# Kernel optimization log

Hardware: AMD Instinct MI355X
Metric: run time of the kernel (lower is better)

## Reference

```python
import jax, jax.numpy as jnp
import numpy as np

B, E, H, LEVELS, MAXN = 16, 256, 256, 12, 2
N = 2 ** LEVELS - 1  # 4095 nodes, level-order perfect binary tree
NODE_VOCAB, EDGE_VOCAB = 64, 128

PARAM_SHAPES = {
    'node_emb': (NODE_VOCAB, E), 'edge_emb': (EDGE_VOCAB, E),
    'bu_Wioux': (E, 3 * H), 'bu_bioux': (3 * H,), 'bu_Wfx': (E, H), 'bu_bfx': (H,),
    'bu_Wiouh': (MAXN * H, 3 * H), 'bu_Wfh': (MAXN, MAXN * H, H),
    'bu_eWih': (E, 4 * H), 'bu_eWhh': (H, 4 * H), 'bu_ebih': (4 * H,), 'bu_ebhh': (4 * H,),
    'td_Wioux': (E, 3 * H), 'td_bioux': (3 * H,), 'td_Wfx': (E, H), 'td_bfx': (H,),
    'td_Wiouhc': (MAXN * H, 3 * H), 'td_Wiouhp': (H, 3 * H),
    'td_Wfchild': (MAXN, (MAXN + 1) * H, H), 'td_Wfparent': ((MAXN + 1) * H, H),
    'td_eWih': (E, 4 * H), 'td_eWhh': (H, 4 * H), 'td_ebih': (4 * H,), 'td_ebhh': (4 * H,),
}
FLOAT_NAMES = list(PARAM_SHAPES)

_sig = jax.nn.sigmoid

def _lstm(x, h, c, Wih, Whh, bih, bhh):
    # torch nn.LSTMCell gate order: i, f, g, o
    g = x @ Wih + h @ Whh + bih + bhh
    i, f, gg, o = jnp.split(g, 4, axis=-1)
    c2 = _sig(f) * c + _sig(i) * jnp.tanh(gg)
    return _sig(o) * jnp.tanh(c2), c2

def _forward(p, node_ids, edge_ids):
    x_all = p['node_emb'][node_ids]  # [B,N,E]
    e_all = p['edge_emb'][edge_ids]  # [B,N,E] edge to parent
    bu_h = [None] * LEVELS
    bu_he = [None] * LEVELS
    bu_ce = [None] * LEVELS
    # ---- bottom-up n-ary TreeLSTM, level by level (deepest first) ----
    for l in range(LEVELS - 1, -1, -1):
        M = 2 ** l
        s = M - 1
        x = x_all[:, s:s + M]
        if l == LEVELS - 1:  # leaves: zero-padded children (no fc terms)
            ch_h = jnp.zeros((B, M, MAXN, H), x.dtype)
            ch_c = ch_h
        else:
            ch_h = bu_he[l + 1].reshape(B, M, MAXN, H)
            ch_c = bu_ce[l + 1].reshape(B, M, MAXN, H)
        cat = ch_h.reshape(B, M, MAXN * H)  # child_cat_h
        iou = x @ p['bu_Wioux'] + p['bu_bioux'] + cat @ p['bu_Wiouh']
        i, o, u = jnp.split(iou, 3, axis=-1)
        i, o, u = _sig(i), _sig(o), jnp.tanh(u)
        fx = x @ p['bu_Wfx'] + p['bu_bfx']
        f = _sig(fx[:, :, None, :] + jnp.einsum('bmc,kch->bmkh', cat, p['bu_Wfh']))
        c = i * u + (f * ch_c).sum(axis=2)
        h = o * jnp.tanh(c)
        bu_h[l] = h
        # edge-transition LSTMCell before passing state to parent
        he, ce = _lstm(e_all[:, s:s + M], h, c, p['bu_eWih'], p['bu_eWhh'], p['bu_ebih'], p['bu_ebhh'])
        bu_he[l] = he
        bu_ce[l] = ce
    # ---- top-down n-ary TreeLSTM (root first) ----
    td_h = [None] * LEVELS
    ph = jnp.zeros((B, 1, H), x_all.dtype)
    pc = ph
    for l in range(LEVELS):
        M = 2 ** l
        s = M - 1
        x = x_all[:, s:s + M]
        if l == LEVELS - 1:
            ch_h = jnp.zeros((B, M, MAXN, H), x.dtype)
            ch_c = ch_h
        else:
            ch_h = bu_he[l + 1].reshape(B, M, MAXN, H)
            ch_c = bu_ce[l + 1].reshape(B, M, MAXN, H)
        cat = ch_h.reshape(B, M, MAXN * H)
        iou = x @ p['td_Wioux'] + p['td_bioux'] + cat @ p['td_Wiouhc'] + ph @ p['td_Wiouhp']
        i, o, u = jnp.split(iou, 3, axis=-1)
        i, o, u = _sig(i), _sig(o), jnp.tanh(u)
        fx = x @ p['td_Wfx'] + p['td_bfx']
        pcat = jnp.concatenate([ph, cat], axis=-1)  # [B,M,(MAXN+1)H]
        f_ch = _sig(fx[:, :, None, :] + jnp.einsum('bmc,kch->bmkh', pcat, p['td_Wfchild']))
        f_par = _sig(fx + pcat @ p['td_Wfparent'])
        c = i * u + (f_ch * ch_c).sum(axis=2) + f_par * pc
        h = o * jnp.tanh(c)
        td_h[l] = h
        if l < LEVELS - 1:
            M2 = 2 * M
            s2 = 2 * M - 1
            ph_r = jnp.repeat(h, 2, axis=1)
            pc_r = jnp.repeat(c, 2, axis=1)
            ph, pc = _lstm(e_all[:, s2:s2 + M2], ph_r, pc_r, p['td_eWih'], p['td_eWhh'], p['td_ebih'], p['td_ebhh'])
    return jnp.concatenate([jnp.concatenate(bu_h, 1), jnp.concatenate(td_h, 1)], axis=-1)  # [B,N,2H]


def setup_inputs() -> dict:
    key = jax.random.key(0)
    ks = jax.random.split(key, len(PARAM_SHAPES) + 2)
    inp = {}
    for k, (name, shp) in zip(ks, PARAM_SHAPES.items()):
        inp[name] = jax.random.normal(k, shp, dtype=jnp.float32) * 0.05
    inp['node_ids'] = jax.random.randint(ks[-2], (B, N), 0, NODE_VOCAB)
    inp['edge_ids'] = jax.random.randint(ks[-1], (B, N), 0, EDGE_VOCAB)
    return inp


def reference(node_emb, edge_emb, bu_Wioux, bu_bioux, bu_Wfx, bu_bfx, bu_Wiouh, bu_Wfh,
              bu_eWih, bu_eWhh, bu_ebih, bu_ebhh, td_Wioux, td_bioux, td_Wfx, td_bfx,
              td_Wiouhc, td_Wiouhp, td_Wfchild, td_Wfparent, td_eWih, td_eWhh, td_ebih, td_ebhh,
              node_ids, edge_ids):
    floats = (node_emb, edge_emb, bu_Wioux, bu_bioux, bu_Wfx, bu_bfx, bu_Wiouh, bu_Wfh,
              bu_eWih, bu_eWhh, bu_ebih, bu_ebhh, td_Wioux, td_bioux, td_Wfx, td_bfx,
              td_Wiouhc, td_Wiouhp, td_Wfchild, td_Wfparent, td_eWih, td_eWhh, td_ebih, td_ebhh)
    return _forward(dict(zip(FLOAT_NAMES, floats)), node_ids, edge_ids)
```

## Files before the change

kernel.cpp:

```cpp
#include <hip/hip_runtime.h>
#include <math.h>

#define NB 16
#define NH 256
#define NLV 12
#define NN 4095
#define OUTW 512

typedef unsigned short u16;
typedef __attribute__((ext_vector_type(4))) float f32x4;
typedef __attribute__((ext_vector_type(8))) short bf16x8;

__device__ __forceinline__ float sigf(float x){ return 1.0f/(1.0f + expf(-x)); }

__device__ __forceinline__ u16 f2bf(float x){
  unsigned int u = __float_as_uint(x);
  return (u16)((u + 0x7fffu + ((u >> 16) & 1u)) >> 16);
}
__device__ __forceinline__ float bf2f(u16 h){
  return __uint_as_float(((unsigned int)h) << 16);
}

__device__ __forceinline__ void gload16(const void* g, void* l){
  __builtin_amdgcn_global_load_lds(
      (const __attribute__((address_space(1))) unsigned int*)g,
      (__attribute__((address_space(3))) unsigned int*)l, 16, 0, 0);
}

template<int VAR, int NG>
__global__ __launch_bounds__(256, (NG >= 5 ? 2 : 3)) void fused_gemm(
    int R, int logM, int s,
    const int* __restrict__ ids,
    const u16* __restrict__ emb,
    const u16* __restrict__ hsrc,
    const u16* __restrict__ hsrc2,
    const u16* __restrict__ Wth, int wstride,
    const float* __restrict__ bias,
    const float* __restrict__ cce,
    const float* __restrict__ cprev,
    float* __restrict__ c_out,
    u16* __restrict__ h_out,
    float* __restrict__ out)
{
  constexpr int K0 = 256;
  constexpr int K1 = (VAR == 0) ? (NG == 5 ? 512 : 0) : 256;
  constexpr int K2 = (VAR == 2 && NG == 6) ? 512 : 0;
  constexpr int KTOT = K0 + K1 + K2;

  __shared__ u16 As[128][64];
  __shared__ u16 Bs[NG * 32][64];

  int tid = threadIdx.x, lane = tid & 63, w = tid >> 6;
  int wrow = w >> 1, whh = w & 1;
  int hh0 = blockIdx.y * 32;
  int M = 1 << logM;

  int lrow8 = lane >> 3;
  int gran  = lane & 7;
  int swz = (gran ^ lrow8) * 8;

  const u16* pa0[4]; const u16* pa1[4]; const u16* pa2[4];
  #pragma unroll
  for (int c = 0; c < 4; ++c){
    int gr = blockIdx.x * 128 + c * 32 + w * 8 + lrow8;
    if (gr > R - 1) gr = R - 1;
    int b = gr >> logM, m = gr & (M - 1);
    int j = s + m;
    pa0[c] = emb + (size_t)ids[b * NN + j] * 256 + swz;
    if constexpr (K1 > 0){
      if constexpr (VAR == 0)
        pa1[c] = hsrc + ((size_t)(b * NN + 2 * j + 1)) * NH + swz;
      else if constexpr (VAR == 3)
        pa1[c] = hsrc + ((size_t)(b * (M >> 1) + (m >> 1))) * NH + swz;
      else
        pa1[c] = hsrc + (size_t)gr * NH + swz;
    }
    if constexpr (K2 > 0)
      pa2[c] = hsrc2 + ((size_t)(b * NN + 2 * j + 1)) * NH + swz;
  }
  const u16* pb = Wth + (size_t)(hh0 + w * 8 + lrow8) * wstride + swz;

  f32x4 acc[NG][4];
  #pragma unroll
  for (int g = 0; g < NG; ++g)
    #pragma unroll
    for (int i = 0; i < 4; ++i) acc[g][i] = (f32x4)0.0f;

  for (int kt = 0; kt < KTOT; kt += 64){
    __syncthreads();
    #pragma unroll
    for (int c = 0; c < 4; ++c){
      const u16* ga;
      if (kt < K0) ga = pa0[c] + kt;
      else if (K1 > 0 && kt < K0 + K1) ga = pa1[c] + (kt - K0);
      else ga = pa2[c] + (kt - K0 - K1);
      gload16(ga, &As[c * 32 + w * 8][0]);
    }
    #pragma unroll
    for (int g = 0; g < NG; ++g)
      gload16(pb + (size_t)g * 256 * wstride + kt, &Bs[g * 32 + w * 8][0]);
    __syncthreads();

    #pragma unroll
    for (int kc = 0; kc < 2; ++kc){
      int g2 = ((kc * 4 + (lane >> 4)) ^ (lane & 7)) * 8;
      bf16x8 a[4];
      #pragma unroll
      for (int i = 0; i < 4; ++i)
        a[i] = *(const bf16x8*)&As[wrow * 64 + i * 16 + (lane & 15)][g2];
      bf16x8 bf[NG];
      #pragma unroll
      for (int g = 0; g < NG; ++g)
        bf[g] = *(const bf16x8*)&Bs[g * 32 + whh * 16 + (lane & 15)][g2];
      #pragma unroll
      for (int g = 0; g < NG; ++g)
        #pragma unroll
        for (int i = 0; i < 4; ++i)
          acc[g][i] = __builtin_amdgcn_mfma_f32_16x16x32_bf16(a[i], bf[g], acc[g][i], 0, 0, 0);
    }
  }

  int hhL = hh0 + whh * 16 + (lane & 15);
  float bb[NG];
  #pragma unroll
  for (int g = 0; g < NG; ++g) bb[g] = bias[g * 256 + hhL];

  #pragma unroll
  for (int i = 0; i < 4; ++i){
    #pragma unroll
    for (int r = 0; r < 4; ++r){
      int row = blockIdx.x * 128 + wrow * 64 + i * 16 + ((lane >> 4) << 2) + r;
      if (row >= R) continue;
      int b = row >> logM, m = row & (M - 1);
      int j = s + m;
      if constexpr (VAR == 0){
        float iv = sigf(acc[0][i][r] + bb[0]);
        float ov = sigf(acc[1][i][r] + bb[1]);
        float uv = tanhf(acc[2][i][r] + bb[2]);
        float c = iv * uv;
        if constexpr (NG == 5){
          float f0 = sigf(acc[3][i][r] + bb[3]);
          float f1 = sigf(acc[4][i][r] + bb[4]);
          c += f0 * cce[((size_t)(b * NN + 2 * j + 1)) * NH + hhL]
             + f1 * cce[((size_t)(b * NN + 2 * j + 2)) * NH + hhL];
        }
        float h = ov * tanhf(c);
        c_out[(size_t)row * NH + hhL] = c;
        h_out[(size_t)row * NH + hhL] = f2bf(h);
        out[((size_t)(b * NN + j)) * OUTW + hhL] = h;
      } else if constexpr (VAR == 1){
        float iv = sigf(acc[0][i][r] + bb[0]);
        float fv = sigf(acc[1][i][r] + bb[1]);
        float gg = tanhf(acc[2][i][r] + bb[2]);
        float ov = sigf(acc[3][i][r] + bb[3]);
        float c2 = fv * cprev[(size_t)row * NH + hhL] + iv * gg;
        float h2 = ov * tanhf(c2);
        size_t di = ((size_t)(b * NN + j)) * NH + hhL;
        h_out[di] = f2bf(h2);
        c_out[di] = c2;
      } else if constexpr (VAR == 2){
        float iv = sigf(acc[0][i][r] + bb[0]);
        float ov = sigf(acc[1][i][r] + bb[1]);
        float uv = tanhf(acc[2][i][r] + bb[2]);
        float fp = sigf(acc[3][i][r] + bb[3]);
        float c = iv * uv + fp * cprev[(size_t)row * NH + hhL];
        if constexpr (NG == 6){
          float f0 = sigf(acc[4][i][r] + bb[4]);
          float f1 = sigf(acc[5][i][r] + bb[5]);
          c += f0 * cce[((size_t)(b * NN + 2 * j + 1)) * NH + hhL]
             + f1 * cce[((size_t)(b * NN + 2 * j + 2)) * NH + hhL];
        }
        float h = ov * tanhf(c);
        c_out[(size_t)row * NH + hhL] = c;
        h_out[(size_t)row * NH + hhL] = f2bf(h);
        out[((size_t)(b * NN + j)) * OUTW + NH + hhL] = h;
      } else {
        float iv = sigf(acc[0][i][r] + bb[0]);
        float fv = sigf(acc[1][i][r] + bb[1]);
        float gg = tanhf(acc[2][i][r] + bb[2]);
        float ov = sigf(acc[3][i][r] + bb[3]);
        int par = b * (M >> 1) + (m >> 1);
        float c2 = fv * cprev[(size_t)par * NH + hhL] + iv * gg;
        float h2 = ov * tanhf(c2);
        h_out[(size_t)row * NH + hhL] = f2bf(h2);
        c_out[(size_t)row * NH + hhL] = c2;
      }
    }
  }
}


__global__ void pack_bu_node_t(const float* __restrict__ Wioux, const float* __restrict__ Wiouh,
                               const float* __restrict__ Wfx, const float* __restrict__ Wfh,
                               const float* __restrict__ bioux, const float* __restrict__ bfx,
                               u16* __restrict__ Wth, float* __restrict__ bd)
{
  int tid = blockIdx.x*256 + threadIdx.x;
  if (tid < 768*1280){
    int n = tid / 768, k = tid % 768;
    float v;
    if (n < 768){
      v = (k < 256) ? Wioux[k*768 + n] : Wiouh[(k-256)*768 + n];
    } else {
      int kidx = (n < 1024) ? 0 : 1;
      int nn = n - 768 - kidx*256;
      v = (k < 256) ? Wfx[k*256 + nn] : Wfh[((size_t)kidx*512 + (k-256))*256 + nn];
    }
    Wth[tid] = f2bf(v);
  }
  if (tid < 1280) bd[tid] = (tid < 768) ? bioux[tid] : bfx[(tid-768) & 255];
}

__global__ void pack_edge_t(const float* __restrict__ Wih, const float* __restrict__ Whh,
                            const float* __restrict__ bih, const float* __restrict__ bhh,
                            u16* __restrict__ Wth, float* __restrict__ bd)
{
  int tid = blockIdx.x*256 + threadIdx.x;
  if (tid < 512*1024){
    int n = tid / 512, k = tid % 512;
    float v = (k < 256) ? Wih[k*1024 + n] : Whh[(k-256)*1024 + n];
    Wth[tid] = f2bf(v);
  }
  if (tid < 1024) bd[tid] = bih[tid] + bhh[tid];
}

__global__ void pack_td_node_t(const float* __restrict__ Wioux, const float* __restrict__ Wiouhc,
                               const float* __restrict__ Wiouhp, const float* __restrict__ Wfx,
                               const float* __restrict__ Wfchild, const float* __restrict__ Wfparent,
                               const float* __restrict__ bioux, const float* __restrict__ bfx,
                               u16* __restrict__ Wth, float* __restrict__ bd)
{
  int tid = blockIdx.x*256 + threadIdx.x;
  if (tid < 1024*1536){
    int n = tid / 1024, k = tid % 1024;
    float v;
    if (n < 768){
      v = (k < 256) ? Wioux[k*768 + n]
        : (k < 512) ? Wiouhp[(k-256)*768 + n]
                    : Wiouhc[(k-512)*768 + n];
    } else if (n < 1024){
      int nn = n - 768;
      v = (k < 256) ? Wfx[k*256 + nn] : Wfparent[(size_t)(k-256)*256 + nn];
    } else {
      int kidx = (n < 1280) ? 0 : 1;
      int nn = n - 1024 - kidx*256;
      v = (k < 256) ? Wfx[k*256 + nn]
                    : Wfchild[((size_t)kidx*768 + (k-256))*256 + nn];
    }
    Wth[tid] = f2bf(v);
  }
  if (tid < 1536) bd[tid] = (tid < 768) ? bioux[tid] : bfx[(tid-768) & 255];
}

__global__ void pack_emb(const float* __restrict__ ne, const float* __restrict__ ee,
                         u16* __restrict__ neb, u16* __restrict__ eeb)
{
  int tid = blockIdx.x*256 + threadIdx.x;
  if (tid < 64*256)  neb[tid] = f2bf(ne[tid]);
  if (tid < 128*256) eeb[tid] = f2bf(ee[tid]);
}

extern "C" void kernel_launch(void* const* d_in, const int* in_sizes, int n_in,
                              void* d_out, int out_size, void* d_ws, size_t ws_size,
                              hipStream_t stream)
{
  const float* node_emb  = (const float*)d_in[0];
  const float* edge_emb  = (const float*)d_in[1];
  const float* bu_Wioux  = (const float*)d_in[2];
  const float* bu_bioux  = (const float*)d_in[3];
  const float* bu_Wfx    = (const float*)d_in[4];
  const float* bu_bfx    = (const float*)d_in[5];
  const float* bu_Wiouh  = (const float*)d_in[6];
  const float* bu_Wfh    = (const float*)d_in[7];
  const float* bu_eWih   = (const float*)d_in[8];
  const float* bu_eWhh   = (const float*)d_in[9];
  const float* bu_ebih   = (const float*)d_in[10];
  const float* bu_ebhh   = (const float*)d_in[11];
  const float* td_Wioux  = (const float*)d_in[12];
  const float* td_bioux  = (const float*)d_in[13];
  const float* td_Wfx    = (const float*)d_in[14];
  const float* td_bfx    = (const float*)d_in[15];
  const float* td_Wiouhc = (const float*)d_in[16];
  const float* td_Wiouhp = (const float*)d_in[17];
  const float* td_Wfchild= (const float*)d_in[18];
  const float* td_Wfparent=(const float*)d_in[19];
  const float* td_eWih   = (const float*)d_in[20];
  const float* td_eWhh   = (const float*)d_in[21];
  const float* td_ebih   = (const float*)d_in[22];
  const float* td_ebhh   = (const float*)d_in[23];
  const int* node_ids    = (const int*)d_in[24];
  const int* edge_ids    = (const int*)d_in[25];
  float* out = (float*)d_out;

  float* fw = (float*)d_ws;
  size_t fo = 0;
  float* bbun = fw + fo; fo += 1280;
  float* bbue = fw + fo; fo += 1024;
  float* btdn = fw + fo; fo += 1536;
  float* btde = fw + fo; fo += 1024;
  float* ce_all = fw + fo; fo += (size_t)NB*NN*NH;
  float* c_lvl  = fw + fo; fo += (size_t)NB*2048*NH;
  float* pc     = fw + fo; fo += (size_t)NB*2048*NH;

  u16* uw = (u16*)(fw + fo);
  size_t uo = 0;
  u16* Wbunh = uw + uo; uo += (size_t)768*1280;
  u16* Wbueh = uw + uo; uo += (size_t)512*1024;
  u16* Wtdnh = uw + uo; uo += (size_t)1024*1536;
  u16* Wtdeh = uw + uo; uo += (size_t)512*1024;
  u16* neb = uw + uo; uo += (size_t)64*256;
  u16* eeb = uw + uo; uo += (size_t)128*256;
  u16* he_b = uw + uo; uo += (size_t)NB*NN*NH;
  u16* hl_b = uw + uo; uo += (size_t)NB*2048*NH;
  u16* ph_b = uw + uo; uo += (size_t)NB*2048*NH;

  pack_bu_node_t<<<(768*1280+255)/256, 256, 0, stream>>>(bu_Wioux, bu_Wiouh, bu_Wfx, bu_Wfh,
      bu_bioux, bu_bfx, Wbunh, bbun);
  pack_edge_t<<<(512*1024+255)/256, 256, 0, stream>>>(bu_eWih, bu_eWhh, bu_ebih, bu_ebhh,
      Wbueh, bbue);
  pack_td_node_t<<<(1024*1536+255)/256, 256, 0, stream>>>(td_Wioux, td_Wiouhc, td_Wiouhp, td_Wfx,
      td_Wfchild, td_Wfparent, td_bioux, td_bfx, Wtdnh, btdn);
  pack_edge_t<<<(512*1024+255)/256, 256, 0, stream>>>(td_eWih, td_eWhh, td_ebih, td_ebhh,
      Wtdeh, btde);
  pack_emb<<<(128*256+255)/256, 256, 0, stream>>>(node_emb, edge_emb, neb, eeb);

  for (int l = NLV-1; l >= 0; --l){
    int M = 1<<l, s = M-1, R = NB*M;
    bool leaf = (l == NLV-1);
    dim3 grid((R + 127) / 128, NH / 32);
    if (leaf){
      fused_gemm<0,3><<<grid, 256, 0, stream>>>(R, l, s, node_ids,
          neb, neb, neb, Wbunh, 768, bbun,
          nullptr, nullptr, c_lvl, hl_b, out);
    } else {
      fused_gemm<0,5><<<grid, 256, 0, stream>>>(R, l, s, node_ids,
          neb, he_b, neb, Wbunh, 768, bbun,
          ce_all, nullptr, c_lvl, hl_b, out);
    }
    fused_gemm<1,4><<<grid, 256, 0, stream>>>(R, l, s, edge_ids,
        eeb, hl_b, neb, Wbueh, 512, bbue,
        nullptr, c_lvl, ce_all, he_b, nullptr);
  }

  hipMemsetAsync(ph_b, 0, (size_t)NB*NH*sizeof(u16), stream);
  hipMemsetAsync(pc, 0, (size_t)NB*NH*sizeof(float), stream);
  for (int l = 0; l < NLV; ++l){
    int M = 1<<l, s = M-1, R = NB*M;
    bool leaf = (l == NLV-1);
    dim3 grid((R + 127) / 128, NH / 32);
    if (!leaf){
      fused_gemm<2,6><<<grid, 256, 0, stream>>>(R, l, s, node_ids,
          neb, ph_b, he_b, Wtdnh, 1024, btdn,
          ce_all, pc, c_lvl, hl_b, out);
      int M2 = 2*M, s2 = 2*M-1, R2 = NB*M2;
      dim3 grid2((R2 + 127) / 128, NH / 32);
      fused_gemm<3,4><<<grid2, 256, 0, stream>>>(R2, l+1, s2, edge_ids,
          eeb, hl_b, neb, Wtdeh, 512, btde,
          nullptr, c_lvl, pc, ph_b, nullptr);
    } else {
      fused_gemm<2,4><<<grid, 256, 0, stream>>>(R, l, s, node_ids,
          neb, ph_b, neb, Wtdnh, 1024, btdn,
          nullptr, pc, c_lvl, hl_b, out);
    }
  }
}
```

Measured before the change: 1.324 ms.

## Fuse small upper tree levels into persistent kernels with grid barriers

Levels 0-7 of both the bottom-up and top-down passes now run inside one persistent kernel each (256 blocks). The kernel loops over tiles and uses a software grid-wide barrier between dependent stages, replacing many tiny kernel launches. The large levels 8-11 still use separate launches. This targets launch overhead and the idle GPU at small levels. In exchange it risks deadlock if not all 256 blocks are co-resident, adds barrier spin cost, and changes launch_bounds occupancy for the NG=5 variant.

```diff
diff --git a/kernel.cpp b/kernel.cpp
--- a/kernel.cpp
+++ b/kernel.cpp
@@ -27,9 +27,27 @@
       (__attribute__((address_space(3))) unsigned int*)l, 16, 0, 0);
 }
 
+__device__ __forceinline__ void grid_bar(int* cnt, int* gen, int nblk){
+  __threadfence();
+  __syncthreads();
+  if (threadIdx.x == 0){
+    int g = __hip_atomic_load(gen, __ATOMIC_RELAXED, __HIP_MEMORY_SCOPE_AGENT);
+    int a = __hip_atomic_fetch_add(cnt, 1, __ATOMIC_ACQ_REL, __HIP_MEMORY_SCOPE_AGENT);
+    if (a == nblk - 1){
+      __hip_atomic_store(cnt, 0, __ATOMIC_RELAXED, __HIP_MEMORY_SCOPE_AGENT);
+      __hip_atomic_fetch_add(gen, 1, __ATOMIC_RELEASE, __HIP_MEMORY_SCOPE_AGENT);
+    } else {
+      while (__hip_atomic_load(gen, __ATOMIC_ACQUIRE, __HIP_MEMORY_SCOPE_AGENT) == g)
+        __builtin_amdgcn_s_sleep(2);
+    }
+  }
+  __syncthreads();
+  __threadfence();
+}
+
 template<int VAR, int NG>
-__global__ __launch_bounds__(256, (NG >= 5 ? 2 : 3)) void fused_gemm(
-    int R, int logM, int s,
+__device__ __forceinline__ void tile_body(
+    int bx, int by, int R, int logM, int s,
     const int* __restrict__ ids,
     const u16* __restrict__ emb,
     const u16* __restrict__ hsrc,
@@ -40,19 +58,17 @@
     const float* __restrict__ cprev,
     float* __restrict__ c_out,
     u16* __restrict__ h_out,
-    float* __restrict__ out)
+    float* __restrict__ out,
+    u16 (*As)[64], u16 (*Bs)[64])
 {
   constexpr int K0 = 256;
   constexpr int K1 = (VAR == 0) ? (NG == 5 ? 512 : 0) : 256;
   constexpr int K2 = (VAR == 2 && NG == 6) ? 512 : 0;
   constexpr int KTOT = K0 + K1 + K2;
 
-  __shared__ u16 As[128][64];
-  __shared__ u16 Bs[NG * 32][64];
-
   int tid = threadIdx.x, lane = tid & 63, w = tid >> 6;
   int wrow = w >> 1, whh = w & 1;
-  int hh0 = blockIdx.y * 32;
+  int hh0 = by * 32;
   int M = 1 << logM;
 
   int lrow8 = lane >> 3;
@@ -62,7 +78,7 @@
   const u16* pa0[4]; const u16* pa1[4]; const u16* pa2[4];
   #pragma unroll
   for (int c = 0; c < 4; ++c){
-    int gr = blockIdx.x * 128 + c * 32 + w * 8 + lrow8;
+    int gr = bx * 128 + c * 32 + w * 8 + lrow8;
     if (gr > R - 1) gr = R - 1;
     int b = gr >> logM, m = gr & (M - 1);
     int j = s + m;
@@ -129,7 +145,7 @@
   for (int i = 0; i < 4; ++i){
     #pragma unroll
     for (int r = 0; r < 4; ++r){
-      int row = blockIdx.x * 128 + wrow * 64 + i * 16 + ((lane >> 4) << 2) + r;
+      int row = bx * 128 + wrow * 64 + i * 16 + ((lane >> 4) << 2) + r;
       if (row >= R) continue;
       int b = row >> logM, m = row & (M - 1);
       int j = s + m;
@@ -189,6 +205,80 @@
   }
 }
 
+template<int VAR, int NG>
+__global__ __launch_bounds__(256, (NG >= 6 ? 2 : 3)) void fused_gemm(
+    int R, int logM, int s,
+    const int* __restrict__ ids,
+    const u16* __restrict__ emb, const u16* __restrict__ hsrc,
+    const u16* __restrict__ hsrc2,
+    const u16* __restrict__ Wth, int wstride,
+    const float* __restrict__ bias,
+    const float* __restrict__ cce, const float* __restrict__ cprev,
+    float* __restrict__ c_out, u16* __restrict__ h_out, float* __restrict__ out)
+{
+  __shared__ u16 As[128][64];
+  __shared__ u16 Bs[NG * 32][64];
+  tile_body<VAR, NG>(blockIdx.x, blockIdx.y, R, logM, s, ids, emb, hsrc, hsrc2,
+                     Wth, wstride, bias, cce, cprev, c_out, h_out, out, As, Bs);
+}
+
+__global__ __launch_bounds__(256, 2) void mega_bu(
+    int* bar,
+    const int* __restrict__ node_ids, const int* __restrict__ edge_ids,
+    const u16* __restrict__ neb, const u16* __restrict__ eeb,
+    const u16* __restrict__ Wbunh, const float* __restrict__ bbun,
+    const u16* __restrict__ Wbueh, const float* __restrict__ bbue,
+    u16* __restrict__ he_b, float* __restrict__ ce_all,
+    float* __restrict__ c_lvl, u16* __restrict__ hl_b,
+    float* __restrict__ out)
+{
+  __shared__ u16 As[128][64];
+  __shared__ u16 Bs[192][64];
+  int nblk = gridDim.x;
+  for (int l = 7; l >= 0; --l){
+    int M = 1 << l, s = M - 1, R = NB * M;
+    int ntiles = ((R + 127) / 128) * 8;
+    for (int t = blockIdx.x; t < ntiles; t += nblk)
+      tile_body<0, 5>(t >> 3, t & 7, R, l, s, node_ids, neb, he_b, he_b,
+                      Wbunh, 768, bbun, ce_all, nullptr, c_lvl, hl_b, out, As, Bs);
+    grid_bar(bar, bar + 1, nblk);
+    for (int t = blockIdx.x; t < ntiles; t += nblk)
+      tile_body<1, 4>(t >> 3, t & 7, R, l, s, edge_ids, eeb, hl_b, nullptr,
+                      Wbueh, 512, bbue, nullptr, c_lvl, ce_all, he_b, nullptr, As, Bs);
+    grid_bar(bar, bar + 1, nblk);
+  }
+}
+
+__global__ __launch_bounds__(256, 2) void mega_td(
+    int* bar,
+    const int* __restrict__ node_ids, const int* __restrict__ edge_ids,
+    const u16* __restrict__ neb, const u16* __restrict__ eeb,
+    const u16* __restrict__ Wtdnh, const float* __restrict__ btdn,
+    const u16* __restrict__ Wtdeh, const float* __restrict__ btde,
+    const u16* __restrict__ he_b, const float* __restrict__ ce_all,
+    float* __restrict__ c_lvl, u16* __restrict__ hl_b,
+    u16* __restrict__ ph_b, float* __restrict__ pc,
+    float* __restrict__ out)
+{
+  __shared__ u16 As[128][64];
+  __shared__ u16 Bs[192][64];
+  int nblk = gridDim.x;
+  for (int l = 0; l <= 7; ++l){
+    int M = 1 << l, s = M - 1, R = NB * M;
+    int ntiles = ((R + 127) / 128) * 8;
+    for (int t = blockIdx.x; t < ntiles; t += nblk)
+      tile_body<2, 6>(t >> 3, t & 7, R, l, s, node_ids, neb, ph_b, he_b,
+                      Wtdnh, 1024, btdn, ce_all, pc, c_lvl, hl_b, out, As, Bs);
+    grid_bar(bar, bar + 1, nblk);
+    int M2 = 2 * M, s2 = 2 * M - 1, R2 = NB * M2;
+    int ntiles2 = ((R2 + 127) / 128) * 8;
+    for (int t = blockIdx.x; t < ntiles2; t += nblk)
+      tile_body<3, 4>(t >> 3, t & 7, R2, l + 1, s2, edge_ids, eeb, hl_b, nullptr,
+                      Wtdeh, 512, btde, nullptr, c_lvl, pc, ph_b, nullptr, As, Bs);
+    grid_bar(bar, bar + 1, nblk);
+  }
+}
+
 
 __global__ void pack_bu_node_t(const float* __restrict__ Wioux, const float* __restrict__ Wiouh,
                                const float* __restrict__ Wfx, const float* __restrict__ Wfh,
@@ -314,6 +404,9 @@
   u16* hl_b = uw + uo; uo += (size_t)NB*2048*NH;
   u16* ph_b = uw + uo; uo += (size_t)NB*2048*NH;
 
+  size_t usedBytes = (fo*sizeof(float) + uo*sizeof(u16) + 255) & ~(size_t)255;
+  int* bar = (int*)((char*)d_ws + usedBytes);
+
   pack_bu_node_t<<<(768*1280+255)/256, 256, 0, stream>>>(bu_Wioux, bu_Wiouh, bu_Wfx, bu_Wfh,
       bu_bioux, bu_bfx, Wbunh, bbun);
   pack_edge_t<<<(512*1024+255)/256, 256, 0, stream>>>(bu_eWih, bu_eWhh, bu_ebih, bu_ebhh,
@@ -324,10 +417,10 @@
       Wtdeh, btde);
   pack_emb<<<(128*256+255)/256, 256, 0, stream>>>(node_emb, edge_emb, neb, eeb);
 
-  for (int l = NLV-1; l >= 0; --l){
+  for (int l = NLV-1; l >= 8; --l){
     int M = 1<<l, s = M-1, R = NB*M;
     bool leaf = (l == NLV-1);
-    dim3 grid((R + 127) / 128, NH / 32);
+    dim3 grid((R + 127) / 128, 8);
     if (leaf){
       fused_gemm<0,3><<<grid, 256, 0, stream>>>(R, l, s, node_ids,
           neb, neb, neb, Wbunh, 768, bbun,
@@ -341,26 +434,33 @@
         eeb, hl_b, neb, Wbueh, 512, bbue,
         nullptr, c_lvl, ce_all, he_b, nullptr);
   }
+  hipMemsetAsync(bar, 0, 16, stream);
+  mega_bu<<<256, 256, 0, stream>>>(bar, node_ids, edge_ids, neb, eeb,
+      Wbunh, bbun, Wbueh, bbue, he_b, ce_all, c_lvl, hl_b, out);
 
   hipMemsetAsync(ph_b, 0, (size_t)NB*NH*sizeof(u16), stream);
   hipMemsetAsync(pc, 0, (size_t)NB*NH*sizeof(float), stream);
-  for (int l = 0; l < NLV; ++l){
+  hipMemsetAsync(bar, 0, 16, stream);
+  mega_td<<<256, 256, 0, stream>>>(bar, node_ids, edge_ids, neb, eeb,
+      Wtdnh, btdn, Wtdeh, btde, he_b, ce_all, c_lvl, hl_b, ph_b, pc, out);
+
+  for (int l = 8; l < NLV; ++l){
     int M = 1<<l, s = M-1, R = NB*M;
     bool leaf = (l == NLV-1);
-    dim3 grid((R + 127) / 128, NH / 32);
-    if (!leaf){
+    dim3 grid((R + 127) / 128, 8);
+    if (leaf){
+      fused_gemm<2,4><<<grid, 256, 0, stream>>>(R, l, s, node_ids,
+          neb, ph_b, neb, Wtdnh, 1024, btdn,
+          nullptr, pc, c_lvl, hl_b, out);
+    } else {
       fused_gemm<2,6><<<grid, 256, 0, stream>>>(R, l, s, node_ids,
           neb, ph_b, he_b, Wtdnh, 1024, btdn,
           ce_all, pc, c_lvl, hl_b, out);
       int M2 = 2*M, s2 = 2*M-1, R2 = NB*M2;
-      dim3 grid2((R2 + 127) / 128, NH / 32);
+      dim3 grid2((R2 + 127) / 128, 8);
       fused_gemm<3,4><<<grid2, 256, 0, stream>>>(R2, l+1, s2, edge_ids,
           eeb, hl_b, neb, Wtdeh, 512, btde,
           nullptr, c_lvl, pc, ph_b, nullptr);
-    } else {
-      fused_gemm<2,4><<<grid, 256, 0, stream>>>(R, l, s, node_ids,
-          neb, ph_b, neb, Wtdnh, 1024, btdn,
-          nullptr, pc, c_lvl, hl_b, out);
-    }
-  }
-}
+    }
+  }
+}
```

Measured after the change: 4.437 ms. 235% more time.
